# Kernel optimization log

Hardware: AMD Instinct MI355X
Metric: run time of the kernel (lower is better)

The kernel has to match this reference:

```python
import jax, jax.numpy as jnp
import numpy as np

D = 1024  # feature_size

def setup_inputs() -> dict:
    key = jax.random.key(0)
    ks = jax.random.split(key, 9)
    s = 1.0 / np.sqrt(D)
    inp = {"x": jax.random.normal(ks[0], (4, 2048, D), dtype=jnp.float32)}
    names = ["Wk", "Wq", "Wv", "Wo"]
    for i, n in enumerate(names):
        inp[n] = jax.random.uniform(ks[1 + 2 * i], (D, D), dtype=jnp.float32, minval=-s, maxval=s)
        inp["b" + n[1]] = jax.random.uniform(ks[2 + 2 * i], (D,), dtype=jnp.float32, minval=-s, maxval=s)
    return inp

def reference(x, Wk, bk, Wq, bq, Wv, bv, Wo, bo):
    # Linear layers: x @ W.T + b (torch nn.Linear convention)
    keys = jnp.einsum('bsd,ed->bse', x, Wk) + bk
    queries = jnp.einsum('bsd,ed->bse', x, Wq) + bq
    values = jnp.einsum('bsd,ed->bse', x, Wv) + bv
    scale = 1.0 / jnp.sqrt(jnp.float32(D))
    scores = jnp.einsum('bqd,bkd->bqk', queries, keys) * scale  # [B,S,S]
    attention = jax.nn.softmax(scores, axis=-1)
    out = jnp.einsum('bqk,bkd->bqd', attention, values)
    out = jnp.einsum('bsd,ed->bse', out, Wo) + bo
    return (out, attention)
```

## Files before the change

### kernel.cpp

```cpp
#include <hip/hip_runtime.h>
#include <hip/hip_bf16.h>


typedef __attribute__((ext_vector_type(8))) _Float16 f16x8;
typedef __attribute__((ext_vector_type(4))) _Float16 f16x4;
typedef __attribute__((ext_vector_type(4))) float f32x4;

static __device__ __forceinline__ void gl_lds16(const void* g, void* s) {
  __builtin_amdgcn_global_load_lds(
      (const __attribute__((address_space(1))) void*)g,
      (__attribute__((address_space(3))) void*)s, 16, 0, 0);
}

__global__ __launch_bounds__(256) void prep(
    const float* __restrict__ x,
    const float* __restrict__ Wq, const float* __restrict__ Wk,
    const float* __restrict__ Wo, const float* __restrict__ Wv,
    const float* __restrict__ bv, const float* __restrict__ bo,
    _Float16* __restrict__ xh, _Float16* __restrict__ Woh,
    _Float16* __restrict__ WvT, _Float16* __restrict__ WqT,
    _Float16* __restrict__ WkT, float* __restrict__ cpb) {
  const int b = blockIdx.x;
  const int tid = threadIdx.x;
  if (b < 8192) {
    const int i = b * 256 + tid;
    float4 v = reinterpret_cast<const float4*>(x)[i];
    f16x4 r = {(_Float16)v.x, (_Float16)v.y, (_Float16)v.z, (_Float16)v.w};
    reinterpret_cast<f16x4*>(xh)[i] = r;
  } else if (b < 9216) {
    const int i = (b - 8192) * 256 + tid;
    float4 v = reinterpret_cast<const float4*>(Wo)[i];
    f16x4 r = {(_Float16)v.x, (_Float16)v.y, (_Float16)v.z, (_Float16)v.w};
    reinterpret_cast<f16x4*>(Woh)[i] = r;
  } else if (b < 9984) {
    const int bb = b - 9216;
    const int which = bb >> 8;
    const float* src = which == 0 ? Wv : which == 1 ? Wq : Wk;
    _Float16* dst = which == 0 ? WvT : which == 1 ? WqT : WkT;
    __shared__ float t[64][65];
    const int tb = bb & 255;
    const int bx = (tb & 15) * 64, by = (tb >> 4) * 64;
    const int tx = tid & 63, ty = tid >> 6;
#pragma unroll
    for (int i = 0; i < 64; i += 4)
      t[ty + i][tx] = src[(long)(by + ty + i) * 1024 + bx + tx];
    __syncthreads();
#pragma unroll
    for (int i = 0; i < 64; i += 4)
      dst[(long)(bx + ty + i) * 1024 + by + tx] = (_Float16)t[tx][ty + i];
  } else {
    const int n = b - 9984;
    float s = 0.f;
    for (int d = tid; d < 1024; d += 256) s += Wo[(long)n * 1024 + d] * bv[d];
#pragma unroll
    for (int o = 32; o >= 1; o >>= 1) s += __shfl_xor(s, o);
    __shared__ float red[4];
    if ((tid & 63) == 0) red[tid >> 6] = s;
    __syncthreads();
    if (tid == 0) cpb[n] = red[0] + red[1] + red[2] + red[3] + bo[n];
  }
}

__global__ __launch_bounds__(256) void wkern(
    const float* __restrict__ bq, const float* __restrict__ bk,
    const _Float16* __restrict__ WkT, const _Float16* __restrict__ WqT,
    float* __restrict__ w1, float* __restrict__ w2, float* __restrict__ c0) {
  const int b = blockIdx.x;
  const int tid = threadIdx.x;
  float s = 0.f;
  if (b < 1024) {
    for (int e = tid; e < 1024; e += 256) s += bq[e] * (float)WkT[(long)b * 1024 + e];
  } else if (b < 2048) {
    const int d = b - 1024;
    for (int e = tid; e < 1024; e += 256) s += bk[e] * (float)WqT[(long)d * 1024 + e];
  } else {
    for (int e = tid; e < 1024; e += 256) s += bq[e] * bk[e];
  }
#pragma unroll
  for (int o = 32; o >= 1; o >>= 1) s += __shfl_xor(s, o);
  __shared__ float red[4];
  if ((tid & 63) == 0) red[tid >> 6] = s;
  __syncthreads();
  if (tid == 0) {
    const float v = red[0] + red[1] + red[2] + red[3];
    if (b < 1024) w1[b] = v;
    else if (b < 2048) w2[b - 1024] = v;
    else c0[0] = v;
  }
}

__global__ __launch_bounds__(256) void rowcol(
    const _Float16* __restrict__ xh, const float* __restrict__ w1,
    const float* __restrict__ w2, const float* __restrict__ c0,
    float* __restrict__ rowb, float* __restrict__ colb) {
  const long i = blockIdx.x;
  const int tid = threadIdx.x;
  f16x4 xv = reinterpret_cast<const f16x4*>(xh + i * 1024)[tid];
  float4 a1 = reinterpret_cast<const float4*>(w1)[tid];
  float4 a2 = reinterpret_cast<const float4*>(w2)[tid];
  float x0 = (float)xv[0], x1 = (float)xv[1], x2 = (float)xv[2], x3 = (float)xv[3];
  float d1 = x0 * a1.x + x1 * a1.y + x2 * a1.z + x3 * a1.w;
  float d2 = x0 * a2.x + x1 * a2.y + x2 * a2.z + x3 * a2.w;
#pragma unroll
  for (int o = 32; o >= 1; o >>= 1) { d1 += __shfl_xor(d1, o); d2 += __shfl_xor(d2, o); }
  __shared__ float r1[4], r2[4];
  if ((tid & 63) == 0) { r1[tid >> 6] = d1; r2[tid >> 6] = d2; }
  __syncthreads();
  if (tid == 0) {
    colb[i] = (r1[0] + r1[1] + r1[2] + r1[3]) * 0.03125f;
    rowb[i] = (r2[0] + r2[1] + r2[2] + r2[3] + c0[0]) * 0.03125f;
  }
}

template <int EPI>
__global__ __launch_bounds__(512, 2) void gemm256p8(
    const _Float16* __restrict__ A, const _Float16* __restrict__ B,
    const float* __restrict__ colb, const float* __restrict__ rowb,
    _Float16* __restrict__ Ch, _Float16* __restrict__ C3,
    int M, int N, int K, long sA, long sB, long sC, float alpha) {
  __shared__ _Float16 lds[2][2][2][8192];

  const unsigned gx = gridDim.x, gy = gridDim.y;
  const unsigned nwg = gx * gy * gridDim.z;
  unsigned flat = (blockIdx.z * gy + blockIdx.y) * gx + blockIdx.x;
  flat = (flat & 7) * (nwg >> 3) + (flat >> 3);
  const long bz = flat / (gx * gy);
  const unsigned rem = flat % (gx * gy);
  const unsigned byi = rem % gy;
  const unsigned bxi = rem / gy;

  const int tid = threadIdx.x;
  const int w = tid >> 6, lane = tid & 63;
  const int wr = w >> 2, wc = w & 3;
  const int lr = lane & 15, q = lane >> 4;
  const long row0 = (long)byi * 256;
  const long col0 = (long)bxi * 256;
  const int nt = K >> 6;

  const _Float16* pA = A + bz * sA;
  const _Float16* pB = B + bz * sB;

  f32x4 acc[8][4] = {};

  const int r0 = tid >> 2, c0i = ((tid & 3) - (r0 >> 1)) & 3;
  const int s1 = tid + 512;
  const int r1 = s1 >> 2, c1 = ((s1 & 3) - (r1 >> 1)) & 3;

  auto stage = [&](int t, int ab, int kk) {
    if (t >= nt) return;
    const int d = t & 1;
    const _Float16* src = ab ? pB : pA;
    const long base = ab ? col0 : row0;
    const long gk = (long)t * 64 + kk * 32;
    gl_lds16(src + (base + r0) * (long)K + gk + c0i * 8, &lds[d][ab][kk][w << 9]);
    gl_lds16(src + (base + r1) * (long)K + gk + c1 * 8,
             &lds[d][ab][kk][4096 + (w << 9)]);
  };
  auto rd = [&](int d, int ab, int kk, int r) -> f16x8 {
    const int slot = (r << 2) + ((q + (r >> 1)) & 3);
    return *(const f16x8*)&lds[d][ab][kk][slot << 3];
  };

#define PH_SYNC()                                         \
  __builtin_amdgcn_s_barrier();                           \
  asm volatile("s_waitcnt lgkmcnt(0)" ::: "memory");      \
  __builtin_amdgcn_sched_barrier(0);                      \
  __builtin_amdgcn_s_setprio(1);
#define PH_END()                                          \
  __builtin_amdgcn_s_setprio(0);                          \
  __builtin_amdgcn_sched_barrier(0);                      \
  __builtin_amdgcn_s_barrier();

  stage(0, 0, 0); stage(0, 1, 0); stage(0, 0, 1); stage(0, 1, 1);
  stage(1, 1, 0); stage(1, 0, 0); stage(1, 1, 1);
  asm volatile("s_waitcnt vmcnt(6)" ::: "memory");
  __builtin_amdgcn_s_barrier();
  __builtin_amdgcn_sched_barrier(0);

  f16x8 a[4], b[4];
  for (int t = 0; t < nt; ++t) {
    const int d = t & 1;
#pragma unroll
    for (int mi = 0; mi < 4; ++mi) a[mi] = rd(d, 0, 0, wr * 128 + mi * 16 + lr);
#pragma unroll
    for (int n = 0; n < 4; ++n) b[n] = rd(d, 1, 0, wc * 64 + n * 16 + lr);
    stage(t + 1, 0, 1);
    PH_SYNC();
#pragma unroll
    for (int mi = 0; mi < 4; ++mi)
#pragma unroll
      for (int n = 0; n < 4; ++n)
        acc[mi][n] = __builtin_amdgcn_mfma_f32_16x16x32_f16(a[mi], b[n], acc[mi][n], 0, 0, 0);
    PH_END();
#pragma unroll
    for (int mi = 0; mi < 4; ++mi) a[mi] = rd(d, 0, 0, wr * 128 + 64 + mi * 16 + lr);
    stage(t + 2, 1, 0);
    PH_SYNC();
#pragma unroll
    for (int mi = 0; mi < 4; ++mi)
#pragma unroll
      for (int n = 0; n < 4; ++n)
        acc[4 + mi][n] = __builtin_amdgcn_mfma_f32_16x16x32_f16(a[mi], b[n], acc[4 + mi][n], 0, 0, 0);
    PH_END();
#pragma unroll
    for (int mi = 0; mi < 4; ++mi) a[mi] = rd(d, 0, 1, wr * 128 + mi * 16 + lr);
#pragma unroll
    for (int n = 0; n < 4; ++n) b[n] = rd(d, 1, 1, wc * 64 + n * 16 + lr);
    stage(t + 2, 0, 0);
    PH_SYNC();
#pragma unroll
    for (int mi = 0; mi < 4; ++mi)
#pragma unroll
      for (int n = 0; n < 4; ++n)
        acc[mi][n] = __builtin_amdgcn_mfma_f32_16x16x32_f16(a[mi], b[n], acc[mi][n], 0, 0, 0);
    PH_END();
#pragma unroll
    for (int mi = 0; mi < 4; ++mi) a[mi] = rd(d, 0, 1, wr * 128 + 64 + mi * 16 + lr);
    stage(t + 2, 1, 1);
    PH_SYNC();
#pragma unroll
    for (int mi = 0; mi < 4; ++mi)
#pragma unroll
      for (int n = 0; n < 4; ++n)
        acc[4 + mi][n] = __builtin_amdgcn_mfma_f32_16x16x32_f16(a[mi], b[n], acc[4 + mi][n], 0, 0, 0);
    __builtin_amdgcn_s_setprio(0);
    __builtin_amdgcn_sched_barrier(0);
    if (t + 2 < nt) asm volatile("s_waitcnt vmcnt(6)" ::: "memory");
    else            asm volatile("s_waitcnt vmcnt(0)" ::: "memory");
    __builtin_amdgcn_s_barrier();
    __builtin_amdgcn_sched_barrier(0);
  }
#undef PH_SYNC
#undef PH_END

  if (EPI == 2) {
#pragma unroll
    for (int mi = 0; mi < 8; ++mi)
#pragma unroll
      for (int n = 0; n < 4; ++n)
#pragma unroll
        for (int r = 0; r < 4; ++r) {
          const long row = row0 + wr * 128 + mi * 16 + q * 4 + r;
          const long col = col0 + wc * 64 + n * 16 + lr;
          float v = acc[mi][n][r] * alpha;
          v += rowb[bz * 2048 + row] + colb[bz * 2048 + col];
          Ch[bz * sC + row * (long)N + col] = (_Float16)v;
        }
  } else {
    if (col0 < 1024) {
#pragma unroll
      for (int mi = 0; mi < 8; ++mi)
#pragma unroll
        for (int n = 0; n < 4; ++n)
#pragma unroll
          for (int r = 0; r < 4; ++r) {
            const long row = row0 + wr * 128 + mi * 16 + q * 4 + r;
            const long col = col0 + wc * 64 + n * 16 + lr;
            Ch[row * 1024 + col] = (_Float16)(acc[mi][n][r] * alpha);
          }
    } else {
      _Float16* wb = ((_Float16*)lds) + w * 4224;
      const long b2 = row0 >> 11;
      const long s2b = (row0 & 2047) + wr * 128;
#pragma unroll
      for (int ch = 0; ch < 2; ++ch) {
#pragma unroll
        for (int nn = 0; nn < 2; ++nn) {
          const int n = ch * 2 + nn;
#pragma unroll
          for (int mi = 0; mi < 8; ++mi)
#pragma unroll
            for (int r = 0; r < 4; ++r) {
              const int cl = nn * 16 + lr;
              const int rl = mi * 16 + q * 4 + r;
              wb[cl * 132 + rl] = (_Float16)(acc[mi][n][r] * alpha);
            }
        }
        asm volatile("s_waitcnt lgkmcnt(0)" ::: "memory");
        __builtin_amdgcn_sched_barrier(0);
        const int cl = lane >> 1, sseg = (lane & 1) * 64;
        _Float16* dst = C3 +
            (b2 * 1024 + (col0 - 1024) + wc * 64 + ch * 32 + cl) * 2048 + s2b + sseg;
        const _Float16* srcp = wb + cl * 132 + sseg;
#pragma unroll
        for (int j = 0; j < 8; ++j)
          *(f16x8*)(dst + j * 8) = *(const f16x8*)(srcp + j * 8);
      }
    }
  }
}

template <int EPI, int BSH>
__global__ __launch_bounds__(256) void gemm128(
    const _Float16* __restrict__ A, const _Float16* __restrict__ B,
    const float* __restrict__ bias, float* __restrict__ Cf,
    _Float16* __restrict__ Ch,
    int M, int N, int K, long sA, long sB, long sC, float alpha, int panelW) {
  __shared__ _Float16 lds[3][2][4096];

  const unsigned gx = gridDim.x, gy = gridDim.y;
  const unsigned nwg = gx * gy * gridDim.z;
  unsigned flat = (blockIdx.z * gy + blockIdx.y) * gx + blockIdx.x;
  flat = (flat & 7) * (nwg >> 3) + (flat >> 3);
  const unsigned pb = gy * panelW;
  const long bz = flat / (gx * gy);
  const unsigned rem = flat % (gx * gy);
  const unsigned pi = rem / pb;
  const unsigned rem2 = rem % pb;
  const unsigned byi = rem2 / panelW;
  const unsigned bxi = pi * panelW + rem2 % panelW;

  const int tid = threadIdx.x;
  const int w = tid >> 6, lane = tid & 63;
  const int wr = w >> 1, wc = w & 1;
  const int lr = lane & 15, q = lane >> 4;
  const long row0 = (long)byi * 128;
  const long col0 = (long)bxi * 128;
  const int nt = K >> 5;

  const _Float16* pA = A + bz * sA;
  const _Float16* pB = BSH ? (B + (row0 >> BSH) * sB) : (B + bz * sB);

  f32x4 acc[4][4] = {};

  const int r0 = tid >> 2, c0i = ((tid & 3) - (r0 >> 1)) & 3;
  const int s1 = tid + 256;
  const int r1 = s1 >> 2, c1 = ((s1 & 3) - (r1 >> 1)) & 3;

  auto stage = [&](int kt) {
    if (kt >= nt) return;
    const int bf = kt % 3;
    const long gk = (long)kt * 32;
#pragma unroll
    for (int ab = 0; ab < 2; ++ab) {
      const _Float16* src = ab ? pB : pA;
      const long base = ab ? col0 : row0;
      gl_lds16(src + (base + r0) * (long)K + gk + c0i * 8, &lds[bf][ab][w << 9]);
      gl_lds16(src + (base + r1) * (long)K + gk + c1 * 8, &lds[bf][ab][2048 + (w << 9)]);
    }
  };
  auto rd = [&](int bf, int ab, int r) -> f16x8 {
    const int slot = (r << 2) + ((q + (r >> 1)) & 3);
    return *(const f16x8*)&lds[bf][ab][slot << 3];
  };

  stage(0); stage(1);
  asm volatile("s_waitcnt vmcnt(4)" ::: "memory");
  __builtin_amdgcn_s_barrier();
  __builtin_amdgcn_sched_barrier(0);

  for (int kt = 0; kt < nt; ++kt) {
    const int bf = kt % 3;
    stage(kt + 2);
    f16x8 a[4], b[4];
#pragma unroll
    for (int m = 0; m < 4; ++m) a[m] = rd(bf, 0, wr * 64 + m * 16 + lr);
#pragma unroll
    for (int n = 0; n < 4; ++n) b[n] = rd(bf, 1, wc * 64 + n * 16 + lr);
#pragma unroll
    for (int m = 0; m < 4; ++m)
#pragma unroll
      for (int n = 0; n < 4; ++n)
        acc[m][n] = __builtin_amdgcn_mfma_f32_16x16x32_f16(a[m], b[n], acc[m][n], 0, 0, 0);
    if (kt < nt - 2) asm volatile("s_waitcnt vmcnt(4)" ::: "memory");
    else             asm volatile("s_waitcnt vmcnt(0)" ::: "memory");
    __builtin_amdgcn_s_barrier();
    __builtin_amdgcn_sched_barrier(0);
  }

#pragma unroll
  for (int m = 0; m < 4; ++m)
#pragma unroll
    for (int n = 0; n < 4; ++n)
#pragma unroll
      for (int r = 0; r < 4; ++r) {
        const long row = row0 + wr * 64 + m * 16 + q * 4 + r;
        const long col = col0 + wc * 64 + n * 16 + lr;
        float v = acc[m][n][r] * alpha;
        if (bias) v += bias[col];
        if (EPI == 0) Cf[bz * sC + row * (long)N + col] = v;
        else          Ch[bz * sC + row * (long)N + col] = (_Float16)v;
      }
}

__global__ __launch_bounds__(256) void softmax16(
    _Float16* __restrict__ Ph, float* __restrict__ attn) {
  const long row = blockIdx.x;
  _Float16* ph = Ph + row * 2048;
  float* ap = attn + row * 2048;
  const int tid = threadIdx.x;
  f16x8 v = reinterpret_cast<const f16x8*>(ph)[tid];
  float x[8];
#pragma unroll
  for (int j = 0; j < 8; ++j) x[j] = (float)v[j];
  float m = x[0];
#pragma unroll
  for (int j = 1; j < 8; ++j) m = fmaxf(m, x[j]);
#pragma unroll
  for (int o = 32; o >= 1; o >>= 1) m = fmaxf(m, __shfl_xor(m, o));
  __shared__ float red[4], red2[4];
  if ((tid & 63) == 0) red[tid >> 6] = m;
  __syncthreads();
  m = fmaxf(fmaxf(red[0], red[1]), fmaxf(red[2], red[3]));
  float s = 0.f;
#pragma unroll
  for (int j = 0; j < 8; ++j) { x[j] = expf(x[j] - m); s += x[j]; }
#pragma unroll
  for (int o = 32; o >= 1; o >>= 1) s += __shfl_xor(s, o);
  if ((tid & 63) == 0) red2[tid >> 6] = s;
  __syncthreads();
  s = red2[0] + red2[1] + red2[2] + red2[3];
  const float inv = 1.0f / s;
#pragma unroll
  for (int j = 0; j < 8; ++j) x[j] *= inv;
  reinterpret_cast<float4*>(ap)[tid * 2] = make_float4(x[0], x[1], x[2], x[3]);
  reinterpret_cast<float4*>(ap)[tid * 2 + 1] = make_float4(x[4], x[5], x[6], x[7]);
  f16x8 pv;
#pragma unroll
  for (int j = 0; j < 8; ++j) pv[j] = (_Float16)x[j];
  reinterpret_cast<f16x8*>(ph)[tid] = pv;
}

extern "C" void kernel_launch(void* const* d_in, const int* in_sizes, int n_in,
                              void* d_out, int out_size, void* d_ws, size_t ws_size,
                              hipStream_t stream) {
  const float* x  = (const float*)d_in[0];
  const float* Wk = (const float*)d_in[1];
  const float* bk = (const float*)d_in[2];
  const float* Wq = (const float*)d_in[3];
  const float* bq = (const float*)d_in[4];
  const float* Wv = (const float*)d_in[5];
  const float* bv = (const float*)d_in[6];
  const float* Wo = (const float*)d_in[7];
  const float* bo = (const float*)d_in[8];

  float* out  = (float*)d_out;
  float* attn = (float*)d_out + 8388608;

  const size_t MB = 1024 * 1024;
  unsigned char* ws = (unsigned char*)d_ws;
  _Float16* xh   = (_Float16*)(ws + 0 * MB);
  _Float16* Wf   = (_Float16*)(ws + 16 * MB);
  _Float16* WkT  = (_Float16*)(ws + 20 * MB);
  _Float16* Woh  = (_Float16*)(ws + 22 * MB);
  _Float16* WqT  = (_Float16*)(ws + 24 * MB);
  _Float16* WvT  = (_Float16*)(ws + 26 * MB);
  float*    rowb = (float*)   (ws + 28 * MB);
  float*    colb = (float*)   (ws + 28 * MB + 32768);
  float*    cpb  = (float*)   (ws + 28 * MB + 65536);
  float*    w1   = (float*)   (ws + 28 * MB + 69632);
  float*    w2   = (float*)   (ws + 28 * MB + 73728);
  float*    c0s  = (float*)   (ws + 28 * MB + 77824);
  _Float16* Y    = (_Float16*)(ws + 29 * MB);
  _Float16* Vt   = (_Float16*)(ws + 45 * MB);
  _Float16* Ph   = (_Float16*)(ws + 61 * MB);

  dim3 blk(256);
  dim3 blk5(512);
  const _Float16* nullh = nullptr;

  hipLaunchKernelGGL(prep, dim3(11008), blk, 0, stream,
                     x, Wq, Wk, Wo, Wv, bv, bo, xh, Woh, WvT, WqT, WkT, cpb);
  hipLaunchKernelGGL(wkern, dim3(2049), blk, 0, stream, bq, bk, WkT, WqT, w1, w2, c0s);
  hipLaunchKernelGGL((gemm128<1, 10>), dim3(8, 16, 1), blk, 0, stream,
                     WkT, WqT, (const float*)nullptr, (float*)nullptr, Wf,
                     2048, 1024, 1024, 0L, 1048576L, 0L, 1.0f, 8);
  hipLaunchKernelGGL(rowcol, dim3(8192), blk, 0, stream, xh, w1, w2, c0s, rowb, colb);
  hipLaunchKernelGGL((gemm256p8<3>), dim3(8, 32, 1), blk5, 0, stream,
                     xh, Wf, (const float*)nullptr, (const float*)nullptr, Y, Vt,
                     8192, 2048, 1024, 0L, 0L, 0L, 1.0f);
  hipLaunchKernelGGL((gemm256p8<2>), dim3(8, 8, 4), blk5, 0, stream,
                     Y, xh, colb, rowb, Ph, (_Float16*)nullh,
                     2048, 2048, 1024, 2097152L, 2097152L, 4194304L, 0.03125f);
  hipLaunchKernelGGL(softmax16, dim3(8192), blk, 0, stream, Ph, attn);
  hipLaunchKernelGGL((gemm128<0, 11>), dim3(8, 64, 1), blk, 0, stream,
                     Ph, Vt, cpb, out, (_Float16*)nullh,
                     8192, 1024, 2048, 0L, 2097152L, 0L, 1.0f, 4);
}
```

Measured before the change: 203.0 us.

## Replace final P·V GEMM with dedicated 128x256 tile, 512-thread pipelined kernel

```diff
diff --git a/kernel.cpp b/kernel.cpp
--- a/kernel.cpp
+++ b/kernel.cpp
@@ -290,6 +290,116 @@
   }
 }
 
+__global__ __launch_bounds__(512, 1) void pv128x256(
+    const _Float16* __restrict__ P, const _Float16* __restrict__ V,
+    const float* __restrict__ cpb, float* __restrict__ out, int K) {
+  __shared__ _Float16 lds[2][2][12288];
+
+  const unsigned gx = gridDim.x, gy = gridDim.y;
+  const unsigned nwg = gx * gy;
+  unsigned flat = blockIdx.y * gx + blockIdx.x;
+  flat = (flat & 7) * (nwg >> 3) + (flat >> 3);
+  const unsigned byi = flat % gy;
+  const unsigned bxi = flat / gy;
+
+  const int tid = threadIdx.x;
+  const int w = tid >> 6, lane = tid & 63;
+  const int wr = w >> 2, wc = w & 3;
+  const int lr = lane & 15, q = lane >> 4;
+  const long row0 = (long)byi * 128;
+  const long col0 = (long)bxi * 256;
+  const int nt = K >> 6;
+
+  const _Float16* pA = P + row0 * (long)K;
+  const _Float16* pB = V + (row0 >> 11) * 2097152L + col0 * (long)K;
+
+  f32x4 acc[4][4] = {};
+
+  const int rA = tid >> 2, cA = ((tid & 3) - (rA >> 1)) & 3;
+  const int sB1 = tid + 512;
+  const int rB1 = sB1 >> 2, cB1 = ((sB1 & 3) - (rB1 >> 1)) & 3;
+
+  auto stage = [&](int t, int kk) {
+    if (t >= nt) return;
+    const int d = t & 1;
+    const long gk = (long)t * 64 + kk * 32;
+    gl_lds16(pA + rA * (long)K + gk + cA * 8, &lds[d][kk][w << 9]);
+    gl_lds16(pB + rA * (long)K + gk + cA * 8, &lds[d][kk][4096 + (w << 9)]);
+    gl_lds16(pB + rB1 * (long)K + gk + cB1 * 8, &lds[d][kk][8192 + (w << 9)]);
+  };
+  auto rdA = [&](int d, int kk, int r) -> f16x8 {
+    const int slot = (r << 2) + ((q + (r >> 1)) & 3);
+    return *(const f16x8*)&lds[d][kk][slot << 3];
+  };
+  auto rdB = [&](int d, int kk, int r) -> f16x8 {
+    const int slot = (r << 2) + ((q + (r >> 1)) & 3);
+    return *(const f16x8*)&lds[d][kk][4096 * 8 / 8 + (slot << 3)];
+  };
+
+#define PH_SYNC()                                         \
+  __builtin_amdgcn_s_barrier();                           \
+  asm volatile("s_waitcnt lgkmcnt(0)" ::: "memory");      \
+  __builtin_amdgcn_sched_barrier(0);                      \
+  __builtin_amdgcn_s_setprio(1);
+
+  stage(0, 0); stage(0, 1); stage(1, 0);
+  asm volatile("s_waitcnt vmcnt(6)" ::: "memory");
+  __builtin_amdgcn_s_barrier();
+  __builtin_amdgcn_sched_barrier(0);
+
+  f16x8 a[4], b[4];
+  for (int t = 0; t < nt; ++t) {
+    const int d = t & 1;
+#pragma unroll
+    for (int mi = 0; mi < 4; ++mi) a[mi] = rdA(d, 0, wr * 64 + mi * 16 + lr);
+#pragma unroll
+    for (int n = 0; n < 4; ++n) b[n] = rdB(d, 0, wc * 64 + n * 16 + lr);
+    stage(t + 1, 1);
+    PH_SYNC();
+#pragma unroll
+    for (int mi = 0; mi < 4; ++mi)
+#pragma unroll
+      for (int n = 0; n < 4; ++n)
+        acc[mi][n] = __builtin_amdgcn_mfma_f32_16x16x32_f16(a[mi], b[n], acc[mi][n], 0, 0, 0);
+    __builtin_amdgcn_s_setprio(0);
+    __builtin_amdgcn_sched_barrier(0);
+    if (t + 1 < nt) asm volatile("s_waitcnt vmcnt(6)" ::: "memory");
+    else            asm volatile("s_waitcnt vmcnt(0)" ::: "memory");
+    __builtin_amdgcn_s_barrier();
+    __builtin_amdgcn_sched_barrier(0);
+#pragma unroll
+    for (int mi = 0; mi < 4; ++mi) a[mi] = rdA(d, 1, wr * 64 + mi * 16 + lr);
+#pragma unroll
+    for (int n = 0; n < 4; ++n) b[n] = rdB(d, 1, wc * 64 + n * 16 + lr);
+    stage(t + 2, 0);
+    PH_SYNC();
+#pragma unroll
+    for (int mi = 0; mi < 4; ++mi)
+#pragma unroll
+      for (int n = 0; n < 4; ++n)
+        acc[mi][n] = __builtin_amdgcn_mfma_f32_16x16x32_f16(a[mi], b[n], acc[mi][n], 0, 0, 0);
+    __builtin_amdgcn_s_setprio(0);
+    __builtin_amdgcn_sched_barrier(0);
+    if (t + 2 < nt)      asm volatile("s_waitcnt vmcnt(6)" ::: "memory");
+    else if (t + 1 < nt) asm volatile("s_waitcnt vmcnt(3)" ::: "memory");
+    else                 asm volatile("s_waitcnt vmcnt(0)" ::: "memory");
+    __builtin_amdgcn_s_barrier();
+    __builtin_amdgcn_sched_barrier(0);
+  }
+#undef PH_SYNC
+
+#pragma unroll
+  for (int mi = 0; mi < 4; ++mi)
+#pragma unroll
+    for (int n = 0; n < 4; ++n)
+#pragma unroll
+      for (int r = 0; r < 4; ++r) {
+        const long row = row0 + wr * 64 + mi * 16 + q * 4 + r;
+        const long col = col0 + wc * 64 + n * 16 + lr;
+        out[row * 1024 + col] = acc[mi][n][r] + cpb[col];
+      }
+}
+
 template <int EPI, int BSH>
 __global__ __launch_bounds__(256) void gemm128(
     const _Float16* __restrict__ A, const _Float16* __restrict__ B,
@@ -473,7 +583,6 @@
                      Y, xh, colb, rowb, Ph, (_Float16*)nullh,
                      2048, 2048, 1024, 2097152L, 2097152L, 4194304L, 0.03125f);
   hipLaunchKernelGGL(softmax16, dim3(8192), blk, 0, stream, Ph, attn);
-  hipLaunchKernelGGL((gemm128<0, 11>), dim3(8, 64, 1), blk, 0, stream,
-                     Ph, Vt, cpb, out, (_Float16*)nullh,
-                     8192, 1024, 2048, 0L, 2097152L, 0L, 1.0f, 4);
-}
+  hipLaunchKernelGGL(pv128x256, dim3(4, 64), blk5, 0, stream,
+                     Ph, Vt, cpb, out, 2048);
+}
```

Measured after the change: 196.8 us. -3.1%, faster.
